# Kernel tuning notes

Measured on AMD Instinct MI355X. Metric: run time of the kernel, lower is better.

Reference implementation:

```python
import jax, jax.numpy as jnp
import numpy as np

THRESH_FACTOR = 0.7  # standard TTQ threshold: 0.7 * mean(|W|)

def ternary_quantize(w):
    delta = THRESH_FACTOR * jnp.mean(jnp.abs(w))
    # {-1, 0, +1} ternary weights
    return jnp.where(w > delta, 1.0, jnp.where(w < -delta, -1.0, 0.0)).astype(w.dtype)

def setup_inputs() -> dict:
    key = jax.random.key(0)
    k1, k2, k3 = jax.random.split(key, 3)
    B, S, D_IN, D_OUT = 8, 4096, 1024, 1024
    inp = {
        "input": jax.random.normal(k1, (B, S, D_IN), dtype=jnp.float32),
        "weight": jax.random.normal(k2, (D_OUT, D_IN), dtype=jnp.float32) * (1.0 / np.sqrt(D_IN)),
        "alpha": jnp.ones((1,), dtype=jnp.float32),
        "bias": jax.random.normal(k3, (D_OUT,), dtype=jnp.float32) * (1.0 / np.sqrt(D_IN)),
    }
    return inp

def reference(input, weight, alpha, bias):
    w_ternary = ternary_quantize(weight)          # [out, in] in {-1,0,1}
    w_eff = w_ternary * alpha                     # scalar alpha scale
    # F.linear: y = x @ W^T + b
    out = jnp.einsum('bsd,od->bso', input, w_eff) + bias
    return out
```

## Files before the change

### kernel.cpp

```cpp
#include <hip/hip_runtime.h>
#include <hip/hip_bf16.h>

typedef __bf16 bf16;
typedef __attribute__((ext_vector_type(8))) __bf16 bf16x8;
typedef __attribute__((ext_vector_type(4))) __bf16 bf16x4;
typedef __attribute__((ext_vector_type(4))) float f32x4;

#define BAR() __builtin_amdgcn_s_barrier()

__device__ __forceinline__ void async_load16(const void* g, void* l) {
    __builtin_amdgcn_global_load_lds(
        (const __attribute__((address_space(1))) void*)g,
        (__attribute__((address_space(3))) void*)l, 16, 0, 0);
}

__global__ __launch_bounds__(256) void k_absconv(const float* __restrict__ w, int wn,
                                                 double* __restrict__ part,
                                                 const float* __restrict__ x,
                                                 bf16* __restrict__ abf, int na8) {
    if (blockIdx.x < 256) {
        __shared__ double sd[256];
        const int per_block = wn / 256;
        const int base = blockIdx.x * per_block;
        double s = 0.0;
        for (int i = threadIdx.x; i < per_block; i += 256)
            s += (double)fabsf(w[base + i]);
        sd[threadIdx.x] = s;
        __syncthreads();
        for (int off = 128; off > 0; off >>= 1) {
            if (threadIdx.x < off) sd[threadIdx.x] += sd[threadIdx.x + off];
            __syncthreads();
        }
        if (threadIdx.x == 0) part[blockIdx.x] = sd[0];
    } else if (abf != nullptr) {
        const int cb     = blockIdx.x - 256;
        const int stride = (gridDim.x - 256) * 256;
        for (int i = cb * 256 + threadIdx.x; i < na8; i += stride) {
            const float4 a = ((const float4*)x)[2 * i];
            const float4 b = ((const float4*)x)[2 * i + 1];
            bf16x8 h;
            h[0] = (bf16)a.x; h[1] = (bf16)a.y; h[2] = (bf16)a.z; h[3] = (bf16)a.w;
            h[4] = (bf16)b.x; h[5] = (bf16)b.y; h[6] = (bf16)b.z; h[7] = (bf16)b.w;
            ((bf16x8*)abf)[i] = h;
        }
    }
}

__global__ __launch_bounds__(256) void k_quantW(const float* __restrict__ w,
                                                const double* __restrict__ part,
                                                bf16* __restrict__ wt, int n4, int wn) {
    __shared__ double sd[256];
    sd[threadIdx.x] = part[threadIdx.x];
    __syncthreads();
    for (int off = 128; off > 0; off >>= 1) {
        if (threadIdx.x < off) sd[threadIdx.x] += sd[threadIdx.x + off];
        __syncthreads();
    }
    const float d = (float)(0.7 * sd[0] / (double)wn);
    const int stride = gridDim.x * 256;
    for (int i = blockIdx.x * 256 + threadIdx.x; i < n4; i += stride) {
        const float4 v = ((const float4*)w)[i];
        bf16x4 o;
        o[0] = (bf16)((v.x > d) ? 1.0f : (v.x < -d) ? -1.0f : 0.0f);
        o[1] = (bf16)((v.y > d) ? 1.0f : (v.y < -d) ? -1.0f : 0.0f);
        o[2] = (bf16)((v.z > d) ? 1.0f : (v.z < -d) ? -1.0f : 0.0f);
        o[3] = (bf16)((v.w > d) ? 1.0f : (v.w < -d) ? -1.0f : 0.0f);
        *(bf16x4*)(wt + (size_t)i * 4) = o;
    }
}

__device__ __forceinline__ void stage_half(const bf16* __restrict__ srch, int K, int kt,
                                           char* dst, int t) {
    #pragma unroll
    for (int r = 0; r < 2; ++r) {
        const int c  = (r << 9) + t;
        const int rp = c >> 3;
        const int s  = (c & 7) ^ ((t >> 3) & 7);
        async_load16(srch + (size_t)rp * K + (kt << 6) + (s << 3), dst + (c << 4));
    }
}

__global__ __launch_bounds__(512, 2) void k_gemm8(const bf16* __restrict__ A,
                                                  const bf16* __restrict__ Bw,
                                                  const float* __restrict__ alphap,
                                                  const float* __restrict__ bias,
                                                  float* __restrict__ C,
                                                  int M, int N, int K) {
    __shared__ __align__(16) char lds[2][2][2][16384];

    const int t    = threadIdx.x;
    const int lane = t & 63;
    const int w    = t >> 6;
    const int wm   = w >> 2;
    const int wn   = w & 3;
    const int lr   = lane & 15;
    const int hi   = lane >> 4;

    const int nbn = N >> 8;
    const int cpx = gridDim.x >> 3;
    const int lid = (blockIdx.x & 7) * cpx + (blockIdx.x >> 3);
    const int bn0 = (lid % nbn) << 8;
    const int bm0 = (lid / nbn) << 8;

    const bf16* Asrc[2] = { A  + (size_t)bm0 * K,  A  + (size_t)(bm0 + 128) * K };
    const bf16* Bsrc[2] = { Bw + (size_t)bn0 * K,  Bw + (size_t)(bn0 + 128) * K };

    f32x4 acc[8][4] = {};
    bf16x8 afq[4][2], bfA[2][2], bfB[2][2];

    const int x0 = ((hi ^ (lr & 7)) << 4);
    const int x1 = (((4 + hi) ^ (lr & 7)) << 4);

#define LDA_Q(MQ, PAR) do { \
    const char* _b = &lds[PAR][0][wm][0]; \
    _Pragma("unroll") \
    for (int m = 0; m < 4; ++m) { \
        const int _r = ((MQ) << 6) + (m << 4) + lr; \
        afq[m][0] = *(const bf16x8*)(_b + _r * 128 + x0); \
        afq[m][1] = *(const bf16x8*)(_b + _r * 128 + x1); \
    } \
} while (0)

#define LDB_Q(DST, NQ, PAR) do { \
    const char* _b = &lds[PAR][1][wn >> 1][0]; \
    _Pragma("unroll") \
    for (int n = 0; n < 2; ++n) { \
        const int _r = ((wn & 1) << 6) + ((((NQ) << 1) + n) << 4) + lr; \
        DST[n][0] = *(const bf16x8*)(_b + _r * 128 + x0); \
        DST[n][1] = *(const bf16x8*)(_b + _r * 128 + x1); \
    } \
} while (0)

#define MF_Q(MQ, NQ, BF) do { \
    __builtin_amdgcn_s_setprio(1); \
    _Pragma("unroll") \
    for (int ks = 0; ks < 2; ++ks) \
        _Pragma("unroll") \
        for (int m = 0; m < 4; ++m) { \
            acc[((MQ)<<2)+m][((NQ)<<1)+0] = __builtin_amdgcn_mfma_f32_16x16x32_bf16(afq[m][ks], BF[0][ks], acc[((MQ)<<2)+m][((NQ)<<1)+0], 0, 0, 0); \
            acc[((MQ)<<2)+m][((NQ)<<1)+1] = __builtin_amdgcn_mfma_f32_16x16x32_bf16(afq[m][ks], BF[1][ks], acc[((MQ)<<2)+m][((NQ)<<1)+1], 0, 0, 0); \
        } \
    __builtin_amdgcn_s_setprio(0); \
} while (0)

#define VMCNT4() asm volatile("s_waitcnt vmcnt(4)" ::: "memory")
#define VMCNT0() asm volatile("s_waitcnt vmcnt(0)" ::: "memory")

    stage_half(Bsrc[0], K, 0, &lds[0][1][0][0], t);
    stage_half(Bsrc[1], K, 0, &lds[0][1][1][0], t);
    stage_half(Asrc[0], K, 0, &lds[0][0][0][0], t);
    stage_half(Asrc[1], K, 0, &lds[0][0][1][0], t);
    stage_half(Bsrc[0], K, 1, &lds[1][1][0][0], t);
    stage_half(Bsrc[1], K, 1, &lds[1][1][1][0], t);
    VMCNT0();
    BAR();

    const int NI = K >> 7;
    for (int i = 0; i < NI; ++i) {
        const int  ktB  = 2 * i + 1;
        const bool last = (i == NI - 1);
        const int  kA2  = 2 * i + 2;
        const int  kB2  = 2 * i + 3;

        VMCNT4();
        LDA_Q(0, 0); LDB_Q(bfA, 0, 0);
        stage_half(Asrc[0], K, ktB, &lds[1][0][0][0], t);
        BAR(); MF_Q(0, 0, bfA); BAR();
        LDB_Q(bfB, 1, 0);
        stage_half(Asrc[1], K, ktB, &lds[1][0][1][0], t);
        BAR(); MF_Q(0, 1, bfB); BAR();
        LDA_Q(1, 0);
        if (!last) stage_half(Bsrc[0], K, kA2, &lds[0][1][0][0], t);
        BAR(); MF_Q(1, 1, bfB); BAR();
        if (!last) stage_half(Bsrc[1], K, kA2, &lds[0][1][1][0], t);
        BAR(); MF_Q(1, 0, bfA); BAR();

        if (last) { VMCNT0(); } else { VMCNT4(); }
        LDA_Q(0, 1); LDB_Q(bfA, 0, 1);
        if (!last) stage_half(Asrc[0], K, kA2, &lds[0][0][0][0], t);
        BAR(); MF_Q(0, 0, bfA); BAR();
        LDB_Q(bfB, 1, 1);
        if (!last) stage_half(Asrc[1], K, kA2, &lds[0][0][1][0], t);
        BAR(); MF_Q(0, 1, bfB); BAR();
        LDA_Q(1, 1);
        if (!last) stage_half(Bsrc[0], K, kB2, &lds[1][1][0][0], t);
        BAR(); MF_Q(1, 1, bfB); BAR();
        if (!last) stage_half(Bsrc[1], K, kB2, &lds[1][1][1][0], t);
        BAR(); MF_Q(1, 0, bfA); BAR();
    }

    const float alpha = *alphap;
    float bv[4];
    #pragma unroll
    for (int nf = 0; nf < 4; ++nf) bv[nf] = bias[bn0 + (wn << 6) + (nf << 4) + lr];

    #pragma unroll
    for (int mf = 0; mf < 8; ++mf) {
        const int grow = bm0 + (wm << 7) + (mf << 4) + (hi << 2);
        #pragma unroll
        for (int nf = 0; nf < 4; ++nf) {
            const int gcol = bn0 + (wn << 6) + (nf << 4) + lr;
            #pragma unroll
            for (int r = 0; r < 4; ++r)
                C[(size_t)(grow + r) * N + gcol] = alpha * acc[mf][nf][r] + bv[nf];
        }
    }
#undef LDA_Q
#undef LDB_Q
#undef MF_Q
#undef VMCNT4
#undef VMCNT0
}

__global__ __launch_bounds__(256) void k_gemm_fb(const float* __restrict__ A,
                                                 const bf16* __restrict__ Bw,
                                                 const float* __restrict__ alphap,
                                                 const float* __restrict__ bias,
                                                 float* __restrict__ C,
                                                 int M, int N, int K) {
    __shared__ bf16 As[128 * 32];
    __shared__ bf16 Bs[128 * 32];
    const int t = threadIdx.x, lane = t & 63, wave = t >> 6;
    const int nbm = M >> 7;
    const int bm0 = (blockIdx.x % nbm) << 7;
    const int bn0 = (blockIdx.x / nbm) << 7;
    const int wr = (wave >> 1) << 6, wc = (wave & 1) << 6;
    f32x4 acc[4][4] = {};
    const int lr = lane & 15, lk = (lane >> 4) << 3;
    for (int k0 = 0; k0 < K; k0 += 32) {
        #pragma unroll
        for (int j = 0; j < 2; ++j) {
            const int c = t + j * 256;
            async_load16(Bw + (size_t)(bn0 + (c >> 2)) * K + k0 + ((c & 3) << 3),
                         (char*)Bs + j * 4096 + wave * 1024);
        }
        #pragma unroll
        for (int i = 0; i < 4; ++i) {
            const int idx = t + i * 256;
            const int row = idx >> 3, c4 = (idx & 7) << 2;
            const float4 v = *(const float4*)(A + (size_t)(bm0 + row) * K + k0 + c4);
            bf16x4 h;
            h[0] = (bf16)v.x; h[1] = (bf16)v.y; h[2] = (bf16)v.z; h[3] = (bf16)v.w;
            *(bf16x4*)(As + row * 32 + c4) = h;
        }
        __syncthreads();
        bf16x8 af[4], bfr[4];
        #pragma unroll
        for (int m = 0; m < 4; ++m) af[m] = *(const bf16x8*)(As + (wr + m * 16 + lr) * 32 + lk);
        #pragma unroll
        for (int n = 0; n < 4; ++n) bfr[n] = *(const bf16x8*)(Bs + (wc + n * 16 + lr) * 32 + lk);
        #pragma unroll
        for (int m = 0; m < 4; ++m)
            #pragma unroll
            for (int n = 0; n < 4; ++n)
                acc[m][n] = __builtin_amdgcn_mfma_f32_16x16x32_bf16(af[m], bfr[n], acc[m][n], 0, 0, 0);
        __syncthreads();
    }
    const float alpha = *alphap;
    #pragma unroll
    for (int m = 0; m < 4; ++m)
        #pragma unroll
        for (int n = 0; n < 4; ++n) {
            const int gcol = bn0 + wc + n * 16 + lr;
            const float bv = bias[gcol];
            #pragma unroll
            for (int r = 0; r < 4; ++r) {
                const int grow = bm0 + wr + m * 16 + ((lane >> 4) << 2) + r;
                C[(size_t)grow * N + gcol] = alpha * acc[m][n][r] + bv;
            }
        }
}

extern "C" void kernel_launch(void* const* d_in, const int* in_sizes, int n_in,
                              void* d_out, int out_size, void* d_ws, size_t ws_size,
                              hipStream_t stream) {
    const float* x     = (const float*)d_in[0];
    const float* wgt   = (const float*)d_in[1];
    const float* alpha = (const float*)d_in[2];
    const float* bias  = (const float*)d_in[3];
    float* out = (float*)d_out;

    const int wn   = in_sizes[1];
    const int dout = in_sizes[3];
    const int din  = wn / dout;
    const int m    = in_sizes[0] / din;

    char* ws = (char*)d_ws;
    double* part = (double*)(ws + 64);
    bf16*   wt   = (bf16*)(ws + 8192);
    bf16*   abf  = (bf16*)(ws + (4u << 20));

    const size_t need = (4u << 20) + (size_t)in_sizes[0] * 2;
    const bool use8 = (ws_size >= need) && (m % 256) == 0 && (dout % 256) == 0 &&
                      (din % 128) == 0 && ((m / 256) * (dout / 256)) % 8 == 0;

    if (use8) {
        k_absconv<<<2304, 256, 0, stream>>>(wgt, wn, part, x, abf, in_sizes[0] / 8);
        k_quantW<<<512, 256, 0, stream>>>(wgt, part, wt, wn / 4, wn);
        dim3 grid((m / 256) * (dout / 256));
        k_gemm8<<<grid, 512, 0, stream>>>(abf, wt, alpha, bias, out, m, dout, din);
    } else {
        k_absconv<<<256, 256, 0, stream>>>(wgt, wn, part, x, nullptr, 0);
        k_quantW<<<512, 256, 0, stream>>>(wgt, part, wt, wn / 4, wn);
        dim3 grid((m / 128) * (dout / 128));
        k_gemm_fb<<<grid, 256, 0, stream>>>(x, wt, alpha, bias, out, m, dout, din);
    }
}
```

Measured before the change: 118.8 us.

## Replace 256x256 double-buffered GEMM with single-buffered 128x256 tile kernel

Replaces the 256x256 tile GEMM, which used 8 waves, a double-buffered 64 KB LDS and an interleaved quarter-tile schedule, with a 128x256 tile kernel. The new kernel uses a single-buffered 48 KB LDS and a simple loop: read fragments, MFMA, then prefetch the next K tile after a barrier. Smaller tiles and fewer accumulator registers are meant to raise occupancy (launch bounds 512,4) and give more blocks across the CUs. The cost is less data reuse per tile, a less overlapped load/compute pipeline, and a full vmcnt(0) wait every iteration.

```diff
diff --git a/kernel.cpp b/kernel.cpp
--- a/kernel.cpp
+++ b/kernel.cpp
@@ -80,13 +80,14 @@
     }
 }
 
-__global__ __launch_bounds__(512, 2) void k_gemm8(const bf16* __restrict__ A,
+__global__ __launch_bounds__(512, 4) void k_gemm2(const bf16* __restrict__ A,
                                                   const bf16* __restrict__ Bw,
                                                   const float* __restrict__ alphap,
                                                   const float* __restrict__ bias,
                                                   float* __restrict__ C,
                                                   int M, int N, int K) {
-    __shared__ __align__(16) char lds[2][2][2][16384];
+    __shared__ __align__(16) char As[16384];
+    __shared__ __align__(16) char Bs[32768];
 
     const int t    = threadIdx.x;
     const int lane = t & 63;
@@ -100,93 +101,70 @@
     const int cpx = gridDim.x >> 3;
     const int lid = (blockIdx.x & 7) * cpx + (blockIdx.x >> 3);
     const int bn0 = (lid % nbn) << 8;
-    const int bm0 = (lid / nbn) << 8;
-
-    const bf16* Asrc[2] = { A  + (size_t)bm0 * K,  A  + (size_t)(bm0 + 128) * K };
-    const bf16* Bsrc[2] = { Bw + (size_t)bn0 * K,  Bw + (size_t)(bn0 + 128) * K };
-
-    f32x4 acc[8][4] = {};
-    bf16x8 afq[4][2], bfA[2][2], bfB[2][2];
+    const int bm0 = (lid / nbn) << 7;
+
+    const bf16* Asrc  = A  + (size_t)bm0 * K;
+    const bf16* Bsrc0 = Bw + (size_t)bn0 * K;
+    const bf16* Bsrc1 = Bw + (size_t)(bn0 + 128) * K;
+
+    f32x4 acc[4][4] = {};
+    bf16x8 af[4], bf[4];
 
     const int x0 = ((hi ^ (lr & 7)) << 4);
     const int x1 = (((4 + hi) ^ (lr & 7)) << 4);
 
-#define LDA_Q(MQ, PAR) do { \
-    const char* _b = &lds[PAR][0][wm][0]; \
+#define RDA(XS) do { \
     _Pragma("unroll") \
     for (int m = 0; m < 4; ++m) { \
-        const int _r = ((MQ) << 6) + (m << 4) + lr; \
-        afq[m][0] = *(const bf16x8*)(_b + _r * 128 + x0); \
-        afq[m][1] = *(const bf16x8*)(_b + _r * 128 + x1); \
+        const int _r = (wm << 6) + (m << 4) + lr; \
+        af[m] = *(const bf16x8*)(As + _r * 128 + (XS)); \
     } \
 } while (0)
 
-#define LDB_Q(DST, NQ, PAR) do { \
-    const char* _b = &lds[PAR][1][wn >> 1][0]; \
+#define RDB(XS) do { \
     _Pragma("unroll") \
-    for (int n = 0; n < 2; ++n) { \
-        const int _r = ((wn & 1) << 6) + ((((NQ) << 1) + n) << 4) + lr; \
-        DST[n][0] = *(const bf16x8*)(_b + _r * 128 + x0); \
-        DST[n][1] = *(const bf16x8*)(_b + _r * 128 + x1); \
+    for (int n = 0; n < 4; ++n) { \
+        const int _r = (wn << 6) + (n << 4) + lr; \
+        bf[n] = *(const bf16x8*)(Bs + _r * 128 + (XS)); \
     } \
 } while (0)
 
-#define MF_Q(MQ, NQ, BF) do { \
+#define MF16() do { \
     __builtin_amdgcn_s_setprio(1); \
     _Pragma("unroll") \
-    for (int ks = 0; ks < 2; ++ks) \
+    for (int m = 0; m < 4; ++m) \
         _Pragma("unroll") \
-        for (int m = 0; m < 4; ++m) { \
-            acc[((MQ)<<2)+m][((NQ)<<1)+0] = __builtin_amdgcn_mfma_f32_16x16x32_bf16(afq[m][ks], BF[0][ks], acc[((MQ)<<2)+m][((NQ)<<1)+0], 0, 0, 0); \
-            acc[((MQ)<<2)+m][((NQ)<<1)+1] = __builtin_amdgcn_mfma_f32_16x16x32_bf16(afq[m][ks], BF[1][ks], acc[((MQ)<<2)+m][((NQ)<<1)+1], 0, 0, 0); \
-        } \
+        for (int n = 0; n < 4; ++n) \
+            acc[m][n] = __builtin_amdgcn_mfma_f32_16x16x32_bf16(af[m], bf[n], acc[m][n], 0, 0, 0); \
     __builtin_amdgcn_s_setprio(0); \
 } while (0)
 
-#define VMCNT4() asm volatile("s_waitcnt vmcnt(4)" ::: "memory")
 #define VMCNT0() asm volatile("s_waitcnt vmcnt(0)" ::: "memory")
-
-    stage_half(Bsrc[0], K, 0, &lds[0][1][0][0], t);
-    stage_half(Bsrc[1], K, 0, &lds[0][1][1][0], t);
-    stage_half(Asrc[0], K, 0, &lds[0][0][0][0], t);
-    stage_half(Asrc[1], K, 0, &lds[0][0][1][0], t);
-    stage_half(Bsrc[0], K, 1, &lds[1][1][0][0], t);
-    stage_half(Bsrc[1], K, 1, &lds[1][1][1][0], t);
+#define LGKM0()  asm volatile("s_waitcnt lgkmcnt(0)" ::: "memory")
+
+    stage_half(Asrc,  K, 0, As, t);
+    stage_half(Bsrc0, K, 0, Bs, t);
+    stage_half(Bsrc1, K, 0, Bs + 16384, t);
     VMCNT0();
     BAR();
 
-    const int NI = K >> 7;
-    for (int i = 0; i < NI; ++i) {
-        const int  ktB  = 2 * i + 1;
-        const bool last = (i == NI - 1);
-        const int  kA2  = 2 * i + 2;
-        const int  kB2  = 2 * i + 3;
-
-        VMCNT4();
-        LDA_Q(0, 0); LDB_Q(bfA, 0, 0);
-        stage_half(Asrc[0], K, ktB, &lds[1][0][0][0], t);
-        BAR(); MF_Q(0, 0, bfA); BAR();
-        LDB_Q(bfB, 1, 0);
-        stage_half(Asrc[1], K, ktB, &lds[1][0][1][0], t);
-        BAR(); MF_Q(0, 1, bfB); BAR();
-        LDA_Q(1, 0);
-        if (!last) stage_half(Bsrc[0], K, kA2, &lds[0][1][0][0], t);
-        BAR(); MF_Q(1, 1, bfB); BAR();
-        if (!last) stage_half(Bsrc[1], K, kA2, &lds[0][1][1][0], t);
-        BAR(); MF_Q(1, 0, bfA); BAR();
-
-        if (last) { VMCNT0(); } else { VMCNT4(); }
-        LDA_Q(0, 1); LDB_Q(bfA, 0, 1);
-        if (!last) stage_half(Asrc[0], K, kA2, &lds[0][0][0][0], t);
-        BAR(); MF_Q(0, 0, bfA); BAR();
-        LDB_Q(bfB, 1, 1);
-        if (!last) stage_half(Asrc[1], K, kA2, &lds[0][0][1][0], t);
-        BAR(); MF_Q(0, 1, bfB); BAR();
-        LDA_Q(1, 1);
-        if (!last) stage_half(Bsrc[0], K, kB2, &lds[1][1][0][0], t);
-        BAR(); MF_Q(1, 1, bfB); BAR();
-        if (!last) stage_half(Bsrc[1], K, kB2, &lds[1][1][1][0], t);
-        BAR(); MF_Q(1, 0, bfA); BAR();
+    const int NT = K >> 6;
+    for (int kt = 0; kt < NT; ++kt) {
+        const bool more = (kt + 1) < NT;
+
+        RDA(x0); RDB(x0);
+        MF16();
+        RDA(x1); RDB(x1);
+        LGKM0();
+        BAR();
+        if (more) {
+            stage_half(Asrc,  K, kt + 1, As, t);
+            stage_half(Bsrc0, K, kt + 1, Bs, t);
+            stage_half(Bsrc1, K, kt + 1, Bs + 16384, t);
+        }
+        MF16();
+        if (more) { VMCNT0(); }
+        BAR();
     }
 
     const float alpha = *alphap;
@@ -195,8 +173,8 @@
     for (int nf = 0; nf < 4; ++nf) bv[nf] = bias[bn0 + (wn << 6) + (nf << 4) + lr];
 
     #pragma unroll
-    for (int mf = 0; mf < 8; ++mf) {
-        const int grow = bm0 + (wm << 7) + (mf << 4) + (hi << 2);
+    for (int mf = 0; mf < 4; ++mf) {
+        const int grow = bm0 + (wm << 6) + (mf << 4) + (hi << 2);
         #pragma unroll
         for (int nf = 0; nf < 4; ++nf) {
             const int gcol = bn0 + (wn << 6) + (nf << 4) + lr;
@@ -205,11 +183,11 @@
                 C[(size_t)(grow + r) * N + gcol] = alpha * acc[mf][nf][r] + bv[nf];
         }
     }
-#undef LDA_Q
-#undef LDB_Q
-#undef MF_Q
-#undef VMCNT4
+#undef RDA
+#undef RDB
+#undef MF16
 #undef VMCNT0
+#undef LGKM0
 }
 
 __global__ __launch_bounds__(256) void k_gemm_fb(const float* __restrict__ A,
@@ -291,14 +269,14 @@
     bf16*   abf  = (bf16*)(ws + (4u << 20));
 
     const size_t need = (4u << 20) + (size_t)in_sizes[0] * 2;
-    const bool use8 = (ws_size >= need) && (m % 256) == 0 && (dout % 256) == 0 &&
-                      (din % 128) == 0 && ((m / 256) * (dout / 256)) % 8 == 0;
-
-    if (use8) {
+    const bool use2 = (ws_size >= need) && (m % 128) == 0 && (dout % 256) == 0 &&
+                      (din % 64) == 0 && ((m / 128) * (dout / 256)) % 8 == 0;
+
+    if (use2) {
         k_absconv<<<2304, 256, 0, stream>>>(wgt, wn, part, x, abf, in_sizes[0] / 8);
         k_quantW<<<512, 256, 0, stream>>>(wgt, part, wt, wn / 4, wn);
-        dim3 grid((m / 256) * (dout / 256));
-        k_gemm8<<<grid, 512, 0, stream>>>(abf, wt, alpha, bias, out, m, dout, din);
+        dim3 grid((m / 128) * (dout / 256));
+        k_gemm2<<<grid, 512, 0, stream>>>(abf, wt, alpha, bias, out, m, dout, din);
     } else {
         k_absconv<<<256, 256, 0, stream>>>(wgt, wn, part, x, nullptr, 0);
         k_quantW<<<512, 256, 0, stream>>>(wgt, part, wt, wn / 4, wn);
```

Result: faster. 115.7 us (median of 2 runs) (-2.6%).
